# Performance work log

Hardware: AMD Instinct MI355X
Metric: run time of the kernel (lower is better)

Reference implementation:

```python
import jax, jax.numpy as jnp
import numpy as np

K = 3          # kernel_size
DEG_P = 6      # numerator coeffs (order 5)
DEG_Q = 4      # denominator coeffs (powers 1..4)


def setup_inputs() -> dict:
    key = jax.random.key(0)
    k1, k2, k3 = jax.random.split(key, 3)
    B, Cin, Cout, H, W = 4, 16, 16, 64, 64
    x = jax.random.normal(k1, (B, Cin, H, W), dtype=jnp.float32)
    # per (out_channel f, in_channel c, kernel position p) rational coefficients
    A = jax.random.normal(k2, (Cout, Cin, K * K, DEG_P), dtype=jnp.float32) * 0.1
    Bc = jax.random.normal(k3, (Cout, Cin, K * K, DEG_Q), dtype=jnp.float32) * 0.1
    return {"x": x, "A": A, "Bc": Bc}


def reference(x, A, Bc):
    # x: [B, C, H, W]; A: [F, C, K*K, 6]; Bc: [F, C, K*K, 4]
    B, C, H, W = x.shape
    pad = (K - 1) // 2
    xp = jnp.pad(x, ((0, 0), (0, 0), (pad, pad), (pad, pad)))
    # sliding windows, one slice per kernel offset -> [K*K, B, C, H, W]
    wins = jnp.stack([xp[:, :, i:i + H, j:j + W]
                      for i in range(K) for j in range(K)])
    # powers x^0..x^5 -> [K*K, B, C, H, W, 6]
    pw = wins[..., None] ** jnp.arange(DEG_P, dtype=x.dtype)
    P = jnp.einsum('pbchwi,fcpi->fpbchw', pw, A)
    Q = 1.0 + jnp.abs(jnp.einsum('pbchwi,fcpi->fpbchw', pw[..., 1:1 + DEG_Q], Bc))
    # sum over kernel positions (p) and input channels (c) -> [F, B, H, W]
    out = jnp.sum(P / Q, axis=(1, 3))
    return jnp.transpose(out, (1, 0, 2, 3))  # [B, F, H, W]
```

## Files before the change

### kernel.cpp

```cpp
#include <hip/hip_runtime.h>


#define BB   4
#define CIN  16
#define COUT 16
#define HH   64
#define WW   64

__global__ __launch_bounds__(256) void KAConv_kernel(
    const float* __restrict__ x,
    const float* __restrict__ A,
    const float* __restrict__ Bc,
    float* __restrict__ out)
{
    const int blk   = blockIdx.x;
    const int f     = blk & 15;
    const int rtile = (blk >> 4) & 7;
    const int b     = blk >> 7;

    const int t    = threadIdx.x;
    const int w    = t & 63;
    const int warp = t >> 6;
    const int r0   = (rtile << 3) + (warp << 1);
    const int r1   = r0 + 1;

    const float* __restrict__ xb = x  + b * (CIN * HH * WW);
    const float* __restrict__ Af = A  + f * (CIN * 9 * 6);
    const float* __restrict__ Bf = Bc + f * (CIN * 9 * 4);

    float acc0 = 0.0f, acc1 = 0.0f;

    for (int c = 0; c < CIN; ++c) {
        const float* __restrict__ xc = xb + c * (HH * WW);

        float vv[4][3];
        #pragma unroll
        for (int ri = 0; ri < 4; ++ri) {
            const int hh  = r0 - 1 + ri;
            const bool okh = (hh >= 0) & (hh < HH);
            #pragma unroll
            for (int j = 0; j < 3; ++j) {
                const int wj = w + j - 1;
                const bool ok = okh & (wj >= 0) & (wj < WW);
                vv[ri][j] = ok ? xc[hh * WW + wj] : 0.0f;
            }
        }

        const float* __restrict__ Ac = Af + c * 54;
        const float* __restrict__ Bq = Bf + c * 36;

        #pragma unroll
        for (int p = 0; p < 9; ++p) {
            const int i = p / 3;
            const int j = p % 3;
            const float va = vv[i][j];
            const float vb = vv[i + 1][j];
            const float* __restrict__ a  = Ac + p * 6;
            const float* __restrict__ bq = Bq + p * 4;

            float P0 = a[5], P1 = a[5];
            P0 = fmaf(P0, va, a[4]);  P1 = fmaf(P1, vb, a[4]);
            P0 = fmaf(P0, va, a[3]);  P1 = fmaf(P1, vb, a[3]);
            P0 = fmaf(P0, va, a[2]);  P1 = fmaf(P1, vb, a[2]);
            P0 = fmaf(P0, va, a[1]);  P1 = fmaf(P1, vb, a[1]);
            P0 = fmaf(P0, va, a[0]);  P1 = fmaf(P1, vb, a[0]);

            float q0 = bq[3], q1 = bq[3];
            q0 = fmaf(q0, va, bq[2]); q1 = fmaf(q1, vb, bq[2]);
            q0 = fmaf(q0, va, bq[1]); q1 = fmaf(q1, vb, bq[1]);
            q0 = fmaf(q0, va, bq[0]); q1 = fmaf(q1, vb, bq[0]);
            q0 *= va;                 q1 *= vb;

            const float d0 = 1.0f + fabsf(q0);
            const float d1 = 1.0f + fabsf(q1);
            acc0 = fmaf(P0, __builtin_amdgcn_rcpf(d0), acc0);
            acc1 = fmaf(P1, __builtin_amdgcn_rcpf(d1), acc1);
        }
    }

    float* __restrict__ of = out + ((b * COUT + f) * HH) * WW + w;
    of[r0 * WW] = acc0;
    of[r1 * WW] = acc1;
}

extern "C" void kernel_launch(void* const* d_in, const int* in_sizes, int n_in,
                              void* d_out, int out_size, void* d_ws, size_t ws_size,
                              hipStream_t stream) {
    const float* x  = (const float*)d_in[0];
    const float* A  = (const float*)d_in[1];
    const float* Bc = (const float*)d_in[2];
    float* out = (float*)d_out;

    const int grid = BB * (HH / 8) * COUT;
    KAConv_kernel<<<grid, 256, 0, stream>>>(x, A, Bc, out);
}
```

Measured before the change: 22.39 us.

## Stage coefficients in LDS, prefetch next channel, and use packed float2 math

Copies the block's A and Bc coefficients into shared memory once per block, so they are no longer read through scalar/global loads inside the loop. Software-prefetches the next input channel's 3x4 window into registers while the current channel is computed. Rewrites the two-row polynomial evaluation with float2 vector types so the compiler can emit packed FMA instructions. This adds register pressure, a block-level barrier, and LDS reads in place of what may have been uniform scalar loads.

```diff
diff --git a/kernel.cpp b/kernel.cpp
--- a/kernel.cpp
+++ b/kernel.cpp
@@ -6,6 +6,26 @@
 #define COUT 16
 #define HH   64
 #define WW   64
+
+typedef float v2f __attribute__((ext_vector_type(2)));
+
+static __device__ __forceinline__ v2f sp(float s) { v2f r; r.x = s; r.y = s; return r; }
+
+static __device__ __forceinline__ void loadw(const float* __restrict__ xb, int c,
+                                             int r0, int w, float v[4][3]) {
+    const float* __restrict__ xc = xb + c * (HH * WW);
+    #pragma unroll
+    for (int ri = 0; ri < 4; ++ri) {
+        const int hh   = r0 - 1 + ri;
+        const bool okh = (hh >= 0) & (hh < HH);
+        #pragma unroll
+        for (int j = 0; j < 3; ++j) {
+            const int wj  = w + j - 1;
+            const bool ok = okh & (wj >= 0) & (wj < WW);
+            v[ri][j] = ok ? xc[hh * WW + wj] : 0.0f;
+        }
+    }
+}
 
 __global__ __launch_bounds__(256) void KAConv_kernel(
     const float* __restrict__ x,
@@ -22,65 +42,72 @@
     const int w    = t & 63;
     const int warp = t >> 6;
     const int r0   = (rtile << 3) + (warp << 1);
-    const int r1   = r0 + 1;
 
-    const float* __restrict__ xb = x  + b * (CIN * HH * WW);
-    const float* __restrict__ Af = A  + f * (CIN * 9 * 6);
-    const float* __restrict__ Bf = Bc + f * (CIN * 9 * 4);
+    __shared__ float sA[CIN * 9 * 6];
+    __shared__ float sB[CIN * 9 * 4];
+    {
+        const float* __restrict__ Af = A  + f * (CIN * 9 * 6);
+        const float* __restrict__ Bf = Bc + f * (CIN * 9 * 4);
+        for (int i = t; i < CIN * 9 * 6; i += 256) sA[i] = Af[i];
+        for (int i = t; i < CIN * 9 * 4; i += 256) sB[i] = Bf[i];
+    }
+    __syncthreads();
 
-    float acc0 = 0.0f, acc1 = 0.0f;
+    const float* __restrict__ xb = x + b * (CIN * HH * WW);
 
+    v2f acc = sp(0.0f);
+
+    float vv[4][3], vn[4][3];
+    loadw(xb, 0, r0, w, vv);
+
+    #pragma unroll 2
     for (int c = 0; c < CIN; ++c) {
-        const float* __restrict__ xc = xb + c * (HH * WW);
+        if (c + 1 < CIN) loadw(xb, c + 1, r0, w, vn);
 
-        float vv[4][3];
-        #pragma unroll
-        for (int ri = 0; ri < 4; ++ri) {
-            const int hh  = r0 - 1 + ri;
-            const bool okh = (hh >= 0) & (hh < HH);
-            #pragma unroll
-            for (int j = 0; j < 3; ++j) {
-                const int wj = w + j - 1;
-                const bool ok = okh & (wj >= 0) & (wj < WW);
-                vv[ri][j] = ok ? xc[hh * WW + wj] : 0.0f;
-            }
-        }
-
-        const float* __restrict__ Ac = Af + c * 54;
-        const float* __restrict__ Bq = Bf + c * 36;
+        const float* __restrict__ Ac = sA + c * 54;
+        const float* __restrict__ Bq = sB + c * 36;
 
         #pragma unroll
         for (int p = 0; p < 9; ++p) {
             const int i = p / 3;
             const int j = p % 3;
-            const float va = vv[i][j];
-            const float vb = vv[i + 1][j];
+            v2f v; v.x = vv[i][j]; v.y = vv[i + 1][j];
+
             const float* __restrict__ a  = Ac + p * 6;
             const float* __restrict__ bq = Bq + p * 4;
 
-            float P0 = a[5], P1 = a[5];
-            P0 = fmaf(P0, va, a[4]);  P1 = fmaf(P1, vb, a[4]);
-            P0 = fmaf(P0, va, a[3]);  P1 = fmaf(P1, vb, a[3]);
-            P0 = fmaf(P0, va, a[2]);  P1 = fmaf(P1, vb, a[2]);
-            P0 = fmaf(P0, va, a[1]);  P1 = fmaf(P1, vb, a[1]);
-            P0 = fmaf(P0, va, a[0]);  P1 = fmaf(P1, vb, a[0]);
+            v2f P = sp(a[5]);
+            P = P * v + sp(a[4]);
+            P = P * v + sp(a[3]);
+            P = P * v + sp(a[2]);
+            P = P * v + sp(a[1]);
+            P = P * v + sp(a[0]);
 
-            float q0 = bq[3], q1 = bq[3];
-            q0 = fmaf(q0, va, bq[2]); q1 = fmaf(q1, vb, bq[2]);
-            q0 = fmaf(q0, va, bq[1]); q1 = fmaf(q1, vb, bq[1]);
-            q0 = fmaf(q0, va, bq[0]); q1 = fmaf(q1, vb, bq[0]);
-            q0 *= va;                 q1 *= vb;
+            v2f q = sp(bq[3]);
+            q = q * v + sp(bq[2]);
+            q = q * v + sp(bq[1]);
+            q = q * v + sp(bq[0]);
+            q = q * v;
 
-            const float d0 = 1.0f + fabsf(q0);
-            const float d1 = 1.0f + fabsf(q1);
-            acc0 = fmaf(P0, __builtin_amdgcn_rcpf(d0), acc0);
-            acc1 = fmaf(P1, __builtin_amdgcn_rcpf(d1), acc1);
+            const float d0 = 1.0f + fabsf(q.x);
+            const float d1 = 1.0f + fabsf(q.y);
+            v2f r; r.x = __builtin_amdgcn_rcpf(d0); r.y = __builtin_amdgcn_rcpf(d1);
+
+            acc += P * r;
+        }
+
+        if (c + 1 < CIN) {
+            #pragma unroll
+            for (int ri = 0; ri < 4; ++ri)
+                #pragma unroll
+                for (int j = 0; j < 3; ++j)
+                    vv[ri][j] = vn[ri][j];
         }
     }
 
     float* __restrict__ of = out + ((b * COUT + f) * HH) * WW + w;
-    of[r0 * WW] = acc0;
-    of[r1 * WW] = acc1;
+    of[r0 * WW]       = acc.x;
+    of[(r0 + 1) * WW] = acc.y;
 }
 
 extern "C" void kernel_launch(void* const* d_in, const int* in_sizes, int n_in,
```

After: 23.65 us. 5.6% more time.

## Split input-channel loop across two thread teams with shared-memory reduction

Applied to the files above, without the earlier changes.

Doubles the block size to 512 threads and splits the 16 input channels into two teams of 8, each accumulating partial sums for the same output pixels. The partials are combined through shared memory after a block barrier, and team 0 writes the result. The goal is to halve the serial per-thread channel loop and expose more parallelism in a grid of only 512 blocks. The cost is a barrier, a shared-memory reduction and idle threads during the final write.

```diff
diff --git a/kernel.cpp b/kernel.cpp
--- a/kernel.cpp
+++ b/kernel.cpp
@@ -7,7 +7,7 @@
 #define HH   64
 #define WW   64
 
-__global__ __launch_bounds__(256) void KAConv_kernel(
+__global__ __launch_bounds__(512, 4) void KAConv_kernel(
     const float* __restrict__ x,
     const float* __restrict__ A,
     const float* __restrict__ Bc,
@@ -18,29 +18,32 @@
     const int rtile = (blk >> 4) & 7;
     const int b     = blk >> 7;
 
-    const int t    = threadIdx.x;
-    const int w    = t & 63;
-    const int warp = t >> 6;
-    const int r0   = (rtile << 3) + (warp << 1);
-    const int r1   = r0 + 1;
+    const int tid  = threadIdx.x;
+    const int team = __builtin_amdgcn_readfirstlane(tid >> 8);
+    const int tp   = tid & 255;
+    const int w    = tp & 63;
+    const int r0   = (rtile << 3) + ((tp >> 6) << 1);
+    const int c0   = team << 3;
 
-    const float* __restrict__ xb = x  + b * (CIN * HH * WW);
-    const float* __restrict__ Af = A  + f * (CIN * 9 * 6);
-    const float* __restrict__ Bf = Bc + f * (CIN * 9 * 4);
+    const float* __restrict__ xb = x  + (b * CIN + c0) * (HH * WW);
+    const float* __restrict__ Af = A  + (f * CIN + c0) * 54;
+    const float* __restrict__ Bf = Bc + (f * CIN + c0) * 36;
+
+    __shared__ float sRed[2 * 256];
 
     float acc0 = 0.0f, acc1 = 0.0f;
 
-    for (int c = 0; c < CIN; ++c) {
+    for (int c = 0; c < 8; ++c) {
         const float* __restrict__ xc = xb + c * (HH * WW);
 
         float vv[4][3];
         #pragma unroll
         for (int ri = 0; ri < 4; ++ri) {
-            const int hh  = r0 - 1 + ri;
+            const int hh   = r0 - 1 + ri;
             const bool okh = (hh >= 0) & (hh < HH);
             #pragma unroll
             for (int j = 0; j < 3; ++j) {
-                const int wj = w + j - 1;
+                const int wj  = w + j - 1;
                 const bool ok = okh & (wj >= 0) & (wj < WW);
                 vv[ri][j] = ok ? xc[hh * WW + wj] : 0.0f;
             }
@@ -78,9 +81,18 @@
         }
     }
 
-    float* __restrict__ of = out + ((b * COUT + f) * HH) * WW + w;
-    of[r0 * WW] = acc0;
-    of[r1 * WW] = acc1;
+    if (team == 1) {
+        sRed[tp]       = acc0;
+        sRed[256 + tp] = acc1;
+    }
+    __syncthreads();
+    if (team == 0) {
+        acc0 += sRed[tp];
+        acc1 += sRed[256 + tp];
+        float* __restrict__ of = out + ((b * COUT + f) * HH) * WW + w;
+        of[r0 * WW]       = acc0;
+        of[(r0 + 1) * WW] = acc1;
+    }
 }
 
 extern "C" void kernel_launch(void* const* d_in, const int* in_sizes, int n_in,
@@ -92,5 +104,5 @@
     float* out = (float*)d_out;
 
     const int grid = BB * (HH / 8) * COUT;
-    KAConv_kernel<<<grid, 256, 0, stream>>>(x, A, Bc, out);
+    KAConv_kernel<<<grid, 512, 0, stream>>>(x, A, Bc, out);
 }
```

After: 20.05 us. 1.12x faster.

## Split input-channel reduction across waves with shared-memory reduction

Applied to the files above, without the earlier changes.

Each block now covers two output rows for one (batch, filter) pair, using 16 waves with one input channel per wave instead of looping over all 16 channels in a single thread. Partial sums go to LDS and are reduced by 128 threads before the store. The aim is to shorten each thread's serial dependency chain and raise parallelism and memory-level parallelism. In exchange it adds a barrier, an LDS reduction step in which only 128 of 1024 threads work, and a larger grid of bigger blocks.

```diff
diff --git a/kernel.cpp b/kernel.cpp
--- a/kernel.cpp
+++ b/kernel.cpp
@@ -7,80 +7,85 @@
 #define HH   64
 #define WW   64
 
-__global__ __launch_bounds__(256) void KAConv_kernel(
+__global__ __launch_bounds__(1024, 8) void KAConv_kernel(
     const float* __restrict__ x,
     const float* __restrict__ A,
     const float* __restrict__ Bc,
     float* __restrict__ out)
 {
-    const int blk   = blockIdx.x;
-    const int f     = blk & 15;
-    const int rtile = (blk >> 4) & 7;
-    const int b     = blk >> 7;
+    const int blk = blockIdx.x;
+    const int f   = blk & 15;
+    const int rp  = (blk >> 4) & 31;
+    const int b   = blk >> 9;
 
-    const int t    = threadIdx.x;
-    const int w    = t & 63;
-    const int warp = t >> 6;
-    const int r0   = (rtile << 3) + (warp << 1);
-    const int r1   = r0 + 1;
+    const int tid  = threadIdx.x;
+    const int cw   = __builtin_amdgcn_readfirstlane(tid >> 6);
+    const int lane = tid & 63;
+    const int w    = lane;
+    const int r0   = rp << 1;
 
-    const float* __restrict__ xb = x  + b * (CIN * HH * WW);
-    const float* __restrict__ Af = A  + f * (CIN * 9 * 6);
-    const float* __restrict__ Bf = Bc + f * (CIN * 9 * 4);
+    const float* __restrict__ Ac = A  + (f * CIN + cw) * 54;
+    const float* __restrict__ Bq = Bc + (f * CIN + cw) * 36;
+    const float* __restrict__ xc = x  + (b * CIN + cw) * (HH * WW);
+
+    float vv[4][3];
+    #pragma unroll
+    for (int ri = 0; ri < 4; ++ri) {
+        const int hh   = r0 - 1 + ri;
+        const bool okh = (hh >= 0) & (hh < HH);
+        #pragma unroll
+        for (int j = 0; j < 3; ++j) {
+            const int wj  = w + j - 1;
+            const bool ok = okh & (wj >= 0) & (wj < WW);
+            vv[ri][j] = ok ? xc[hh * WW + wj] : 0.0f;
+        }
+    }
 
     float acc0 = 0.0f, acc1 = 0.0f;
 
-    for (int c = 0; c < CIN; ++c) {
-        const float* __restrict__ xc = xb + c * (HH * WW);
+    #pragma unroll
+    for (int p = 0; p < 9; ++p) {
+        const int i = p / 3;
+        const int j = p % 3;
+        const float va = vv[i][j];
+        const float vb = vv[i + 1][j];
+        const float a0 = Ac[p * 6 + 0], a1 = Ac[p * 6 + 1], a2 = Ac[p * 6 + 2];
+        const float a3 = Ac[p * 6 + 3], a4 = Ac[p * 6 + 4], a5 = Ac[p * 6 + 5];
+        const float b1 = Bq[p * 4 + 0], b2 = Bq[p * 4 + 1];
+        const float b3 = Bq[p * 4 + 2], b4 = Bq[p * 4 + 3];
 
-        float vv[4][3];
-        #pragma unroll
-        for (int ri = 0; ri < 4; ++ri) {
-            const int hh  = r0 - 1 + ri;
-            const bool okh = (hh >= 0) & (hh < HH);
-            #pragma unroll
-            for (int j = 0; j < 3; ++j) {
-                const int wj = w + j - 1;
-                const bool ok = okh & (wj >= 0) & (wj < WW);
-                vv[ri][j] = ok ? xc[hh * WW + wj] : 0.0f;
-            }
-        }
+        float P0 = a5, P1 = a5;
+        P0 = fmaf(P0, va, a4);  P1 = fmaf(P1, vb, a4);
+        P0 = fmaf(P0, va, a3);  P1 = fmaf(P1, vb, a3);
+        P0 = fmaf(P0, va, a2);  P1 = fmaf(P1, vb, a2);
+        P0 = fmaf(P0, va, a1);  P1 = fmaf(P1, vb, a1);
+        P0 = fmaf(P0, va, a0);  P1 = fmaf(P1, vb, a0);
 
-        const float* __restrict__ Ac = Af + c * 54;
-        const float* __restrict__ Bq = Bf + c * 36;
+        float q0 = b4, q1 = b4;
+        q0 = fmaf(q0, va, b3);  q1 = fmaf(q1, vb, b3);
+        q0 = fmaf(q0, va, b2);  q1 = fmaf(q1, vb, b2);
+        q0 = fmaf(q0, va, b1);  q1 = fmaf(q1, vb, b1);
+        q0 *= va;               q1 *= vb;
 
-        #pragma unroll
-        for (int p = 0; p < 9; ++p) {
-            const int i = p / 3;
-            const int j = p % 3;
-            const float va = vv[i][j];
-            const float vb = vv[i + 1][j];
-            const float* __restrict__ a  = Ac + p * 6;
-            const float* __restrict__ bq = Bq + p * 4;
-
-            float P0 = a[5], P1 = a[5];
-            P0 = fmaf(P0, va, a[4]);  P1 = fmaf(P1, vb, a[4]);
-            P0 = fmaf(P0, va, a[3]);  P1 = fmaf(P1, vb, a[3]);
-            P0 = fmaf(P0, va, a[2]);  P1 = fmaf(P1, vb, a[2]);
-            P0 = fmaf(P0, va, a[1]);  P1 = fmaf(P1, vb, a[1]);
-            P0 = fmaf(P0, va, a[0]);  P1 = fmaf(P1, vb, a[0]);
-
-            float q0 = bq[3], q1 = bq[3];
-            q0 = fmaf(q0, va, bq[2]); q1 = fmaf(q1, vb, bq[2]);
-            q0 = fmaf(q0, va, bq[1]); q1 = fmaf(q1, vb, bq[1]);
-            q0 = fmaf(q0, va, bq[0]); q1 = fmaf(q1, vb, bq[0]);
-            q0 *= va;                 q1 *= vb;
-
-            const float d0 = 1.0f + fabsf(q0);
-            const float d1 = 1.0f + fabsf(q1);
-            acc0 = fmaf(P0, __builtin_amdgcn_rcpf(d0), acc0);
-            acc1 = fmaf(P1, __builtin_amdgcn_rcpf(d1), acc1);
-        }
+        const float d0 = 1.0f + fabsf(q0);
+        const float d1 = 1.0f + fabsf(q1);
+        acc0 = fmaf(P0, __builtin_amdgcn_rcpf(d0), acc0);
+        acc1 = fmaf(P1, __builtin_amdgcn_rcpf(d1), acc1);
     }
 
-    float* __restrict__ of = out + ((b * COUT + f) * HH) * WW + w;
-    of[r0 * WW] = acc0;
-    of[r1 * WW] = acc1;
+    __shared__ float sRed[CIN][128];
+    sRed[cw][lane]      = acc0;
+    sRed[cw][64 + lane] = acc1;
+    __syncthreads();
+
+    if (tid < 128) {
+        float s = 0.0f;
+        #pragma unroll
+        for (int k = 0; k < CIN; ++k) s += sRed[k][tid];
+        const int row = r0 + (tid >> 6);
+        const int col = tid & 63;
+        out[((b * COUT + f) * HH + row) * WW + col] = s;
+    }
 }
 
 extern "C" void kernel_launch(void* const* d_in, const int* in_sizes, int n_in,
@@ -91,6 +96,6 @@
     const float* Bc = (const float*)d_in[2];
     float* out = (float*)d_out;
 
-    const int grid = BB * (HH / 8) * COUT;
-    KAConv_kernel<<<grid, 256, 0, stream>>>(x, A, Bc, out);
+    const int grid = BB * (HH / 2) * COUT;
+    KAConv_kernel<<<grid, 1024, 0, stream>>>(x, A, Bc, out);
 }
```

Result: faster. 19.97 us (-10.8%).
